# Kernel optimization log

Measured on AMD Instinct MI355X. Metric: run time of the kernel, lower is better.

Reference implementation:

```python
import jax, jax.numpy as jnp
import numpy as np

N = 100_000      # nodes
E = 1_600_000    # edges (avg degree 16)
DN = 64          # node feature dim
DE = 64          # edge feature dim


def _w(k, shape):
    fan_in = shape[0]
    return jax.random.normal(k, shape, dtype=jnp.float32) / np.sqrt(fan_in)


def setup_inputs() -> dict:
    key = jax.random.key(0)
    ks = jax.random.split(key, 12)
    x = jax.random.normal(ks[0], (N, DN), dtype=jnp.float32)
    e = jax.random.normal(ks[1], (E, DE), dtype=jnp.float32)
    senders = jax.random.randint(ks[2], (E,), 0, N)
    receivers = jax.random.randint(ks[3], (E,), 0, N)
    return {
        "x": x, "e": e, "senders": senders, "receivers": receivers,
        "We1": _w(ks[4], (DE + 2 * DN, DE)), "be1": jnp.zeros((DE,), jnp.float32),
        "We2": _w(ks[5], (DE, DE)),          "be2": jnp.zeros((DE,), jnp.float32),
        "We3": _w(ks[6], (DE, DE)),          "be3": jnp.zeros((DE,), jnp.float32),
        "Wn1": _w(ks[7], (DN + DE, DN)),     "bn1": jnp.zeros((DN,), jnp.float32),
        "Wn2": _w(ks[8], (DN, DN)),          "bn2": jnp.zeros((DN,), jnp.float32),
        "Wn3": _w(ks[9], (DN, DN)),          "bn3": jnp.zeros((DN,), jnp.float32),
    }


def reference(x, e, senders, receivers,
              We1, be1, We2, be2, We3, be3,
              Wn1, bn1, Wn2, bn2, Wn3, bn3):
    # --- EdgeBlock: concat(edge, sender, receiver) -> MLP ---
    h = jnp.concatenate([e, x[senders], x[receivers]], axis=-1)  # [E, DE+2*DN]
    h = jax.nn.relu(h @ We1 + be1)
    h = jax.nn.relu(h @ We2 + be2)
    e_new = h @ We3 + be3                                        # [E, DE]
    # --- NodeBlock: sum-aggregate receiving edges, concat(node, agg) -> MLP ---
    agg = jax.ops.segment_sum(e_new, receivers, num_segments=N)  # [N, DE]
    g = jnp.concatenate([x, agg], axis=-1)                       # [N, DN+DE]
    g = jax.nn.relu(g @ Wn1 + bn1)
    g = jax.nn.relu(g @ Wn2 + bn2)
    x_new = g @ Wn3 + bn3                                        # [N, DN]
    return x_new
```

## Files before the change

### kernel.cpp

```cpp
#include <hip/hip_runtime.h>

#define NN 100000
#define NE 1600000

typedef short v8s __attribute__((ext_vector_type(8)));
typedef float v4f __attribute__((ext_vector_type(4)));
typedef unsigned short v4u16 __attribute__((ext_vector_type(4)));

__device__ __forceinline__ unsigned short f2bf(float f) {
    union { float f; unsigned int u; } v; v.f = f;
    unsigned int r = v.u + 0x7FFFu + ((v.u >> 16) & 1u);
    return (unsigned short)(r >> 16);
}

__device__ __forceinline__ void store_bf4(unsigned short* base, int row, int k, float4 v) {
    v4u16 p;
    p.x = f2bf(v.x); p.y = f2bf(v.y); p.z = f2bf(v.z); p.w = f2bf(v.w);
    *(v4u16*)(base + ((k >> 5) * 2048 + row * 32 + (k & 31))) = p;
}

#define MFMA16(acc, a, b) acc = __builtin_amdgcn_mfma_f32_16x16x32_bf16(a, b, acc, 0, 0, 0)

__global__ __launch_bounds__(256, 2) void edge_kernel(
    const float* __restrict__ x, const float* __restrict__ e,
    const int* __restrict__ snd, const int* __restrict__ rcv,
    const float* __restrict__ We1, const float* __restrict__ be1,
    const float* __restrict__ We2, const float* __restrict__ be2,
    const float* __restrict__ We3, const float* __restrict__ be3,
    float* agg, int numTiles)
{
    extern __shared__ unsigned short smem[];
    unsigned short* WT1 = smem;
    unsigned short* WT2 = WT1 + 12288;
    unsigned short* WT3 = WT2 + 4096;
    unsigned short* A   = WT3 + 4096;

    const int tid = threadIdx.x;

    for (int idx = tid; idx < 192 * 64; idx += 256) {
        int k = idx >> 6, n = idx & 63;
        WT1[(k >> 5) * 2048 + n * 32 + (k & 31)] = f2bf(We1[idx]);
    }
    for (int idx = tid; idx < 64 * 64; idx += 256) {
        int k = idx >> 6, n = idx & 63;
        int off = (k >> 5) * 2048 + n * 32 + (k & 31);
        WT2[off] = f2bf(We2[idx]);
        WT3[off] = f2bf(We3[idx]);
    }

    const int lane = tid & 63;
    const int wv   = tid >> 6;
    const int l15  = lane & 15;
    const int quad = lane >> 4;
    const int astrip = wv * 16;

    float b1v[4], b2v[4], b3v[4];
#pragma unroll
    for (int nt = 0; nt < 4; ++nt) {
        b1v[nt] = be1[nt * 16 + l15];
        b2v[nt] = be2[nt * 16 + l15];
        b3v[nt] = be3[nt * 16 + l15];
    }

    const int arow = (astrip + l15) * 32 + quad * 8;
    const int brow = l15 * 32 + quad * 8;

    __syncthreads();

    for (int tile = blockIdx.x; tile < numTiles; tile += gridDim.x) {
        const int ebase = tile * 64;

#pragma unroll
        for (int t = 0; t < 4; ++t) {
            int idx = tid + t * 256;
            int row = idx >> 4;
            int k0  = (idx & 15) * 4;
            float4 ve = *(const float4*)(e + (size_t)(ebase + row) * 64 + k0);
            store_bf4(A, row, k0, ve);
            int s = snd[ebase + row];
            float4 vs = *(const float4*)(x + (size_t)s * 64 + k0);
            store_bf4(A, row, 64 + k0, vs);
            int r = rcv[ebase + row];
            float4 vr = *(const float4*)(x + (size_t)r * 64 + k0);
            store_bf4(A, row, 128 + k0, vr);
        }
        __syncthreads();

        {
            v4f acc[4];
#pragma unroll
            for (int nt = 0; nt < 4; ++nt) acc[nt] = (v4f){0.f, 0.f, 0.f, 0.f};
#pragma unroll
            for (int kb = 0; kb < 6; ++kb) {
                v8s af = *(const v8s*)(A + kb * 2048 + arow);
#pragma unroll
                for (int nt = 0; nt < 4; ++nt) {
                    v8s bf = *(const v8s*)(WT1 + kb * 2048 + brow + nt * 512);
                    MFMA16(acc[nt], af, bf);
                }
            }
#pragma unroll
            for (int nt = 0; nt < 4; ++nt) {
                int kk = nt * 16 + l15;
#pragma unroll
                for (int r = 0; r < 4; ++r) {
                    int m = astrip + quad * 4 + r;
                    float v = acc[nt][r] + b1v[nt];
                    v = v > 0.f ? v : 0.f;
                    A[(kk >> 5) * 2048 + m * 32 + (kk & 31)] = f2bf(v);
                }
            }
        }

        {
            v4f acc[4];
#pragma unroll
            for (int nt = 0; nt < 4; ++nt) acc[nt] = (v4f){0.f, 0.f, 0.f, 0.f};
#pragma unroll
            for (int kb = 0; kb < 2; ++kb) {
                v8s af = *(const v8s*)(A + kb * 2048 + arow);
#pragma unroll
                for (int nt = 0; nt < 4; ++nt) {
                    v8s bf = *(const v8s*)(WT2 + kb * 2048 + brow + nt * 512);
                    MFMA16(acc[nt], af, bf);
                }
            }
#pragma unroll
            for (int nt = 0; nt < 4; ++nt) {
                int kk = nt * 16 + l15;
#pragma unroll
                for (int r = 0; r < 4; ++r) {
                    int m = astrip + quad * 4 + r;
                    float v = acc[nt][r] + b2v[nt];
                    v = v > 0.f ? v : 0.f;
                    A[(2 + (kk >> 5)) * 2048 + m * 32 + (kk & 31)] = f2bf(v);
                }
            }
        }

        {
            v4f acc[4];
#pragma unroll
            for (int nt = 0; nt < 4; ++nt) acc[nt] = (v4f){0.f, 0.f, 0.f, 0.f};
#pragma unroll
            for (int kb = 0; kb < 2; ++kb) {
                v8s af = *(const v8s*)(A + (2 + kb) * 2048 + arow);
#pragma unroll
                for (int nt = 0; nt < 4; ++nt) {
                    v8s bf = *(const v8s*)(WT3 + kb * 2048 + brow + nt * 512);
                    MFMA16(acc[nt], af, bf);
                }
            }
#pragma unroll
            for (int r = 0; r < 4; ++r) {
                int el = astrip + quad * 4 + r;
                int dst = rcv[ebase + el];
                float* aggrow = agg + (size_t)dst * 64;
#pragma unroll
                for (int nt = 0; nt < 4; ++nt) {
                    unsafeAtomicAdd(aggrow + nt * 16 + l15, acc[nt][r] + b3v[nt]);
                }
            }
        }
        __syncthreads();
    }
}

__global__ __launch_bounds__(256, 2) void node_kernel(
    const float* __restrict__ x,
    const float* __restrict__ Wn1, const float* __restrict__ bn1,
    const float* __restrict__ Wn2, const float* __restrict__ bn2,
    const float* __restrict__ Wn3, const float* __restrict__ bn3,
    float* aggout)
{
    extern __shared__ unsigned short smem[];
    unsigned short* WT1 = smem;
    unsigned short* WT2 = WT1 + 8192;
    unsigned short* WT3 = WT2 + 4096;
    unsigned short* A   = WT3 + 4096;

    const int tid = threadIdx.x;

    for (int idx = tid; idx < 128 * 64; idx += 256) {
        int k = idx >> 6, n = idx & 63;
        WT1[(k >> 5) * 2048 + n * 32 + (k & 31)] = f2bf(Wn1[idx]);
    }
    for (int idx = tid; idx < 64 * 64; idx += 256) {
        int k = idx >> 6, n = idx & 63;
        int off = (k >> 5) * 2048 + n * 32 + (k & 31);
        WT2[off] = f2bf(Wn2[idx]);
        WT3[off] = f2bf(Wn3[idx]);
    }

    const int lane = tid & 63;
    const int wv   = tid >> 6;
    const int l15  = lane & 15;
    const int quad = lane >> 4;
    const int astrip = wv * 16;

    float b1v[4], b2v[4], b3v[4];
#pragma unroll
    for (int nt = 0; nt < 4; ++nt) {
        b1v[nt] = bn1[nt * 16 + l15];
        b2v[nt] = bn2[nt * 16 + l15];
        b3v[nt] = bn3[nt * 16 + l15];
    }

    const int arow = (astrip + l15) * 32 + quad * 8;
    const int brow = l15 * 32 + quad * 8;
    const int nbase = blockIdx.x * 64;

    __syncthreads();

#pragma unroll
    for (int t = 0; t < 4; ++t) {
        int idx = tid + t * 256;
        int row = idx >> 4;
        int k0  = (idx & 15) * 4;
        int node = nbase + row;
        float4 vx = {0.f, 0.f, 0.f, 0.f}, va = {0.f, 0.f, 0.f, 0.f};
        if (node < NN) {
            vx = *(const float4*)(x + (size_t)node * 64 + k0);
            va = *(const float4*)(aggout + (size_t)node * 64 + k0);
        }
        store_bf4(A, row, k0, vx);
        store_bf4(A, row, 64 + k0, va);
    }
    __syncthreads();

    {
        v4f acc[4];
#pragma unroll
        for (int nt = 0; nt < 4; ++nt) acc[nt] = (v4f){0.f, 0.f, 0.f, 0.f};
#pragma unroll
        for (int kb = 0; kb < 4; ++kb) {
            v8s af = *(const v8s*)(A + kb * 2048 + arow);
#pragma unroll
            for (int nt = 0; nt < 4; ++nt) {
                v8s bf = *(const v8s*)(WT1 + kb * 2048 + brow + nt * 512);
                MFMA16(acc[nt], af, bf);
            }
        }
#pragma unroll
        for (int nt = 0; nt < 4; ++nt) {
            int kk = nt * 16 + l15;
#pragma unroll
            for (int r = 0; r < 4; ++r) {
                int m = astrip + quad * 4 + r;
                float v = acc[nt][r] + b1v[nt];
                v = v > 0.f ? v : 0.f;
                A[(kk >> 5) * 2048 + m * 32 + (kk & 31)] = f2bf(v);
            }
        }
    }

    {
        v4f acc[4];
#pragma unroll
        for (int nt = 0; nt < 4; ++nt) acc[nt] = (v4f){0.f, 0.f, 0.f, 0.f};
#pragma unroll
        for (int kb = 0; kb < 2; ++kb) {
            v8s af = *(const v8s*)(A + kb * 2048 + arow);
#pragma unroll
            for (int nt = 0; nt < 4; ++nt) {
                v8s bf = *(const v8s*)(WT2 + kb * 2048 + brow + nt * 512);
                MFMA16(acc[nt], af, bf);
            }
        }
#pragma unroll
        for (int nt = 0; nt < 4; ++nt) {
            int kk = nt * 16 + l15;
#pragma unroll
            for (int r = 0; r < 4; ++r) {
                int m = astrip + quad * 4 + r;
                float v = acc[nt][r] + b2v[nt];
                v = v > 0.f ? v : 0.f;
                A[(2 + (kk >> 5)) * 2048 + m * 32 + (kk & 31)] = f2bf(v);
            }
        }
    }

    {
        v4f acc[4];
#pragma unroll
        for (int nt = 0; nt < 4; ++nt) acc[nt] = (v4f){0.f, 0.f, 0.f, 0.f};
#pragma unroll
        for (int kb = 0; kb < 2; ++kb) {
            v8s af = *(const v8s*)(A + (2 + kb) * 2048 + arow);
#pragma unroll
            for (int nt = 0; nt < 4; ++nt) {
                v8s bf = *(const v8s*)(WT3 + kb * 2048 + brow + nt * 512);
                MFMA16(acc[nt], af, bf);
            }
        }
#pragma unroll
        for (int r = 0; r < 4; ++r) {
            int node = nbase + astrip + quad * 4 + r;
            if (node < NN) {
#pragma unroll
                for (int nt = 0; nt < 4; ++nt) {
                    aggout[(size_t)node * 64 + nt * 16 + l15] = acc[nt][r] + b3v[nt];
                }
            }
        }
    }
}

extern "C" void kernel_launch(void* const* d_in, const int* in_sizes, int n_in,
                              void* d_out, int out_size, void* d_ws, size_t ws_size,
                              hipStream_t stream) {
    const float* x   = (const float*)d_in[0];
    const float* e   = (const float*)d_in[1];
    const int*   snd = (const int*)d_in[2];
    const int*   rcv = (const int*)d_in[3];
    const float* We1 = (const float*)d_in[4];  const float* be1 = (const float*)d_in[5];
    const float* We2 = (const float*)d_in[6];  const float* be2 = (const float*)d_in[7];
    const float* We3 = (const float*)d_in[8];  const float* be3 = (const float*)d_in[9];
    const float* Wn1 = (const float*)d_in[10]; const float* bn1 = (const float*)d_in[11];
    const float* Wn2 = (const float*)d_in[12]; const float* bn2 = (const float*)d_in[13];
    const float* Wn3 = (const float*)d_in[14]; const float* bn3 = (const float*)d_in[15];
    float* out = (float*)d_out;

    hipMemsetAsync(out, 0, (size_t)NN * 64 * sizeof(float), stream);

    edge_kernel<<<512, 256, 65536, stream>>>(x, e, snd, rcv,
                                             We1, be1, We2, be2, We3, be3,
                                             out, NE / 64);

    node_kernel<<<(NN + 63) / 64, 256, 49152, stream>>>(x,
                                                        Wn1, bn1, Wn2, bn2, Wn3, bn3,
                                                        out);
}
```

Measured before the change: 874.6 us.

## Sort edges by receiver, swizzle LDS, keep small weights in registers, persistent node kernel

Adds a counting-sort pass (count, single-block scan, fill) that builds a receiver-sorted permutation. The edge kernel walks edges through this permutation and merges runs of equal receivers before issuing atomics, which cuts atomic traffic. LDS tiles get an XOR swizzle to avoid bank conflicts. The 64x64 layer-2/3 weights move into registers to shrink LDS and raise occupancy to 3 blocks. The node kernel becomes persistent. In exchange, edge feature reads are now gathered through the permutation, and the preprocessing adds extra launches, including a serial single-block scan.

```diff
diff --git a/kernel.cpp b/kernel.cpp
--- a/kernel.cpp
+++ b/kernel.cpp
@@ -13,39 +13,76 @@
     return (unsigned short)(r >> 16);
 }
 
+__device__ __forceinline__ int swz_p(int row, int p) {
+    return (p & 7) | (((((p >> 3) ^ (row >> 1))) & 3) << 3);
+}
+
 __device__ __forceinline__ void store_bf4(unsigned short* base, int row, int k, float4 v) {
     v4u16 p;
     p.x = f2bf(v.x); p.y = f2bf(v.y); p.z = f2bf(v.z); p.w = f2bf(v.w);
-    *(v4u16*)(base + ((k >> 5) * 2048 + row * 32 + (k & 31))) = p;
+    *(v4u16*)(base + ((k >> 5) * 2048 + row * 32 + swz_p(row, k & 31))) = p;
 }
 
 #define MFMA16(acc, a, b) acc = __builtin_amdgcn_mfma_f32_16x16x32_bf16(a, b, acc, 0, 0, 0)
 
-__global__ __launch_bounds__(256, 2) void edge_kernel(
+__global__ void count_kernel(const int* __restrict__ rcv, int* cnt) {
+    int i = blockIdx.x * 256 + threadIdx.x;
+    if (i < NE) atomicAdd(&cnt[rcv[i]], 1);
+}
+
+__global__ void scan_kernel(const int* __restrict__ cnt, int* cur) {
+    __shared__ int wsum[16];
+    __shared__ int carry_s;
+    const int tid = threadIdx.x;
+    const int lane = tid & 63, w = tid >> 6;
+    if (tid == 0) carry_s = 0;
+    __syncthreads();
+    for (int base = 0; base < NN; base += 1024) {
+        int i = base + tid;
+        int v = (i < NN) ? cnt[i] : 0;
+        int s = v;
+#pragma unroll
+        for (int off = 1; off < 64; off <<= 1) {
+            int t = __shfl_up(s, off, 64);
+            if (lane >= off) s += t;
+        }
+        if (lane == 63) wsum[w] = s;
+        __syncthreads();
+        int woff = 0;
+        for (int j = 0; j < w; ++j) woff += wsum[j];
+        int carry = carry_s;
+        __syncthreads();
+        if (i < NN) cur[i] = carry + woff + s - v;
+        if (tid == 1023) carry_s = carry + woff + s;
+        __syncthreads();
+    }
+}
+
+__global__ void fill_kernel(const int* __restrict__ rcv, int* cur, int* perm) {
+    int i = blockIdx.x * 256 + threadIdx.x;
+    if (i < NE) {
+        int p = atomicAdd(&cur[rcv[i]], 1);
+        perm[p] = i;
+    }
+}
+
+__global__ __launch_bounds__(256, 3) void edge_kernel(
     const float* __restrict__ x, const float* __restrict__ e,
     const int* __restrict__ snd, const int* __restrict__ rcv,
     const float* __restrict__ We1, const float* __restrict__ be1,
     const float* __restrict__ We2, const float* __restrict__ be2,
     const float* __restrict__ We3, const float* __restrict__ be3,
-    float* agg, int numTiles)
+    const int* __restrict__ perm, float* agg, int numTiles)
 {
     extern __shared__ unsigned short smem[];
     unsigned short* WT1 = smem;
-    unsigned short* WT2 = WT1 + 12288;
-    unsigned short* WT3 = WT2 + 4096;
-    unsigned short* A   = WT3 + 4096;
+    unsigned short* A   = smem + 12288;
 
     const int tid = threadIdx.x;
 
     for (int idx = tid; idx < 192 * 64; idx += 256) {
         int k = idx >> 6, n = idx & 63;
-        WT1[(k >> 5) * 2048 + n * 32 + (k & 31)] = f2bf(We1[idx]);
-    }
-    for (int idx = tid; idx < 64 * 64; idx += 256) {
-        int k = idx >> 6, n = idx & 63;
-        int off = (k >> 5) * 2048 + n * 32 + (k & 31);
-        WT2[off] = f2bf(We2[idx]);
-        WT3[off] = f2bf(We3[idx]);
+        WT1[(k >> 5) * 2048 + n * 32 + swz_p(n, k & 31)] = f2bf(We1[idx]);
     }
 
     const int lane = tid & 63;
@@ -54,6 +91,23 @@
     const int quad = lane >> 4;
     const int astrip = wv * 16;
 
+    v8s w2f[2][4], w3f[2][4];
+#pragma unroll
+    for (int kb = 0; kb < 2; ++kb)
+#pragma unroll
+        for (int nt = 0; nt < 4; ++nt) {
+            int n = nt * 16 + l15;
+            v8s f2, f3;
+#pragma unroll
+            for (int j = 0; j < 8; ++j) {
+                int k = kb * 32 + quad * 8 + j;
+                f2[j] = (short)f2bf(We2[k * 64 + n]);
+                f3[j] = (short)f2bf(We3[k * 64 + n]);
+            }
+            w2f[kb][nt] = f2;
+            w3f[kb][nt] = f3;
+        }
+
     float b1v[4], b2v[4], b3v[4];
 #pragma unroll
     for (int nt = 0; nt < 4; ++nt) {
@@ -62,8 +116,14 @@
         b3v[nt] = be3[nt * 16 + l15];
     }
 
-    const int arow = (astrip + l15) * 32 + quad * 8;
-    const int brow = l15 * 32 + quad * 8;
+    const int amrow = astrip + l15;
+    const int aoff  = amrow * 32 + (((quad ^ (amrow >> 1)) & 3) << 3);
+    int boff[4];
+#pragma unroll
+    for (int nt = 0; nt < 4; ++nt) {
+        int n = nt * 16 + l15;
+        boff[nt] = n * 32 + (((quad ^ (n >> 1)) & 3) << 3);
+    }
 
     __syncthreads();
 
@@ -75,12 +135,13 @@
             int idx = tid + t * 256;
             int row = idx >> 4;
             int k0  = (idx & 15) * 4;
-            float4 ve = *(const float4*)(e + (size_t)(ebase + row) * 64 + k0);
+            int eid = perm ? perm[ebase + row] : (ebase + row);
+            float4 ve = *(const float4*)(e + (size_t)eid * 64 + k0);
             store_bf4(A, row, k0, ve);
-            int s = snd[ebase + row];
+            int s = snd[eid];
             float4 vs = *(const float4*)(x + (size_t)s * 64 + k0);
             store_bf4(A, row, 64 + k0, vs);
-            int r = rcv[ebase + row];
+            int r = rcv[eid];
             float4 vr = *(const float4*)(x + (size_t)r * 64 + k0);
             store_bf4(A, row, 128 + k0, vr);
         }
@@ -92,10 +153,10 @@
             for (int nt = 0; nt < 4; ++nt) acc[nt] = (v4f){0.f, 0.f, 0.f, 0.f};
 #pragma unroll
             for (int kb = 0; kb < 6; ++kb) {
-                v8s af = *(const v8s*)(A + kb * 2048 + arow);
+                v8s af = *(const v8s*)(A + kb * 2048 + aoff);
 #pragma unroll
                 for (int nt = 0; nt < 4; ++nt) {
-                    v8s bf = *(const v8s*)(WT1 + kb * 2048 + brow + nt * 512);
+                    v8s bf = *(const v8s*)(WT1 + kb * 2048 + boff[nt]);
                     MFMA16(acc[nt], af, bf);
                 }
             }
@@ -107,7 +168,7 @@
                     int m = astrip + quad * 4 + r;
                     float v = acc[nt][r] + b1v[nt];
                     v = v > 0.f ? v : 0.f;
-                    A[(kk >> 5) * 2048 + m * 32 + (kk & 31)] = f2bf(v);
+                    A[(kk >> 5) * 2048 + m * 32 + swz_p(m, kk & 31)] = f2bf(v);
                 }
             }
         }
@@ -118,12 +179,9 @@
             for (int nt = 0; nt < 4; ++nt) acc[nt] = (v4f){0.f, 0.f, 0.f, 0.f};
 #pragma unroll
             for (int kb = 0; kb < 2; ++kb) {
-                v8s af = *(const v8s*)(A + kb * 2048 + arow);
-#pragma unroll
-                for (int nt = 0; nt < 4; ++nt) {
-                    v8s bf = *(const v8s*)(WT2 + kb * 2048 + brow + nt * 512);
-                    MFMA16(acc[nt], af, bf);
-                }
+                v8s af = *(const v8s*)(A + kb * 2048 + aoff);
+#pragma unroll
+                for (int nt = 0; nt < 4; ++nt) MFMA16(acc[nt], af, w2f[kb][nt]);
             }
 #pragma unroll
             for (int nt = 0; nt < 4; ++nt) {
@@ -133,7 +191,7 @@
                     int m = astrip + quad * 4 + r;
                     float v = acc[nt][r] + b2v[nt];
                     v = v > 0.f ? v : 0.f;
-                    A[(2 + (kk >> 5)) * 2048 + m * 32 + (kk & 31)] = f2bf(v);
+                    A[(2 + (kk >> 5)) * 2048 + m * 32 + swz_p(m, kk & 31)] = f2bf(v);
                 }
             }
         }
@@ -144,52 +202,61 @@
             for (int nt = 0; nt < 4; ++nt) acc[nt] = (v4f){0.f, 0.f, 0.f, 0.f};
 #pragma unroll
             for (int kb = 0; kb < 2; ++kb) {
-                v8s af = *(const v8s*)(A + (2 + kb) * 2048 + arow);
-#pragma unroll
-                for (int nt = 0; nt < 4; ++nt) {
-                    v8s bf = *(const v8s*)(WT3 + kb * 2048 + brow + nt * 512);
-                    MFMA16(acc[nt], af, bf);
-                }
-            }
+                v8s af = *(const v8s*)(A + (2 + kb) * 2048 + aoff);
+#pragma unroll
+                for (int nt = 0; nt < 4; ++nt) MFMA16(acc[nt], af, w3f[kb][nt]);
+            }
+            int dsts[4];
 #pragma unroll
             for (int r = 0; r < 4; ++r) {
                 int el = astrip + quad * 4 + r;
-                int dst = rcv[ebase + el];
-                float* aggrow = agg + (size_t)dst * 64;
-#pragma unroll
-                for (int nt = 0; nt < 4; ++nt) {
-                    unsafeAtomicAdd(aggrow + nt * 16 + l15, acc[nt][r] + b3v[nt]);
-                }
-            }
-        }
-        __syncthreads();
-    }
-}
-
-__global__ __launch_bounds__(256, 2) void node_kernel(
+                int eid = perm ? perm[ebase + el] : (ebase + el);
+                dsts[r] = rcv[eid];
+            }
+            float sum[4];
+            int cur = dsts[0];
+#pragma unroll
+            for (int nt = 0; nt < 4; ++nt) sum[nt] = acc[nt][0] + b3v[nt];
+#pragma unroll
+            for (int r = 1; r < 4; ++r) {
+                if (dsts[r] == cur) {
+#pragma unroll
+                    for (int nt = 0; nt < 4; ++nt) sum[nt] += acc[nt][r] + b3v[nt];
+                } else {
+                    float* aggrow = agg + (size_t)cur * 64;
+#pragma unroll
+                    for (int nt = 0; nt < 4; ++nt)
+                        unsafeAtomicAdd(aggrow + nt * 16 + l15, sum[nt]);
+                    cur = dsts[r];
+#pragma unroll
+                    for (int nt = 0; nt < 4; ++nt) sum[nt] = acc[nt][r] + b3v[nt];
+                }
+            }
+            float* aggrow = agg + (size_t)cur * 64;
+#pragma unroll
+            for (int nt = 0; nt < 4; ++nt)
+                unsafeAtomicAdd(aggrow + nt * 16 + l15, sum[nt]);
+        }
+        __syncthreads();
+    }
+}
+
+__global__ __launch_bounds__(256, 3) void node_kernel(
     const float* __restrict__ x,
     const float* __restrict__ Wn1, const float* __restrict__ bn1,
     const float* __restrict__ Wn2, const float* __restrict__ bn2,
     const float* __restrict__ Wn3, const float* __restrict__ bn3,
-    float* aggout)
+    float* aggout, int numTiles)
 {
     extern __shared__ unsigned short smem[];
     unsigned short* WT1 = smem;
-    unsigned short* WT2 = WT1 + 8192;
-    unsigned short* WT3 = WT2 + 4096;
-    unsigned short* A   = WT3 + 4096;
+    unsigned short* A   = smem + 8192;
 
     const int tid = threadIdx.x;
 
     for (int idx = tid; idx < 128 * 64; idx += 256) {
         int k = idx >> 6, n = idx & 63;
-        WT1[(k >> 5) * 2048 + n * 32 + (k & 31)] = f2bf(Wn1[idx]);
-    }
-    for (int idx = tid; idx < 64 * 64; idx += 256) {
-        int k = idx >> 6, n = idx & 63;
-        int off = (k >> 5) * 2048 + n * 32 + (k & 31);
-        WT2[off] = f2bf(Wn2[idx]);
-        WT3[off] = f2bf(Wn3[idx]);
+        WT1[(k >> 5) * 2048 + n * 32 + swz_p(n, k & 31)] = f2bf(Wn1[idx]);
     }
 
     const int lane = tid & 63;
@@ -198,6 +265,23 @@
     const int quad = lane >> 4;
     const int astrip = wv * 16;
 
+    v8s w2f[2][4], w3f[2][4];
+#pragma unroll
+    for (int kb = 0; kb < 2; ++kb)
+#pragma unroll
+        for (int nt = 0; nt < 4; ++nt) {
+            int n = nt * 16 + l15;
+            v8s f2, f3;
+#pragma unroll
+            for (int j = 0; j < 8; ++j) {
+                int k = kb * 32 + quad * 8 + j;
+                f2[j] = (short)f2bf(Wn2[k * 64 + n]);
+                f3[j] = (short)f2bf(Wn3[k * 64 + n]);
+            }
+            w2f[kb][nt] = f2;
+            w3f[kb][nt] = f3;
+        }
+
     float b1v[4], b2v[4], b3v[4];
 #pragma unroll
     for (int nt = 0; nt < 4; ++nt) {
@@ -206,103 +290,106 @@
         b3v[nt] = bn3[nt * 16 + l15];
     }
 
-    const int arow = (astrip + l15) * 32 + quad * 8;
-    const int brow = l15 * 32 + quad * 8;
-    const int nbase = blockIdx.x * 64;
+    const int amrow = astrip + l15;
+    const int aoff  = amrow * 32 + (((quad ^ (amrow >> 1)) & 3) << 3);
+    int boff[4];
+#pragma unroll
+    for (int nt = 0; nt < 4; ++nt) {
+        int n = nt * 16 + l15;
+        boff[nt] = n * 32 + (((quad ^ (n >> 1)) & 3) << 3);
+    }
 
     __syncthreads();
 
-#pragma unroll
-    for (int t = 0; t < 4; ++t) {
-        int idx = tid + t * 256;
-        int row = idx >> 4;
-        int k0  = (idx & 15) * 4;
-        int node = nbase + row;
-        float4 vx = {0.f, 0.f, 0.f, 0.f}, va = {0.f, 0.f, 0.f, 0.f};
-        if (node < NN) {
-            vx = *(const float4*)(x + (size_t)node * 64 + k0);
-            va = *(const float4*)(aggout + (size_t)node * 64 + k0);
-        }
-        store_bf4(A, row, k0, vx);
-        store_bf4(A, row, 64 + k0, va);
-    }
-    __syncthreads();
-
-    {
-        v4f acc[4];
-#pragma unroll
-        for (int nt = 0; nt < 4; ++nt) acc[nt] = (v4f){0.f, 0.f, 0.f, 0.f};
-#pragma unroll
-        for (int kb = 0; kb < 4; ++kb) {
-            v8s af = *(const v8s*)(A + kb * 2048 + arow);
+    for (int tile = blockIdx.x; tile < numTiles; tile += gridDim.x) {
+        const int nbase = tile * 64;
+
+#pragma unroll
+        for (int t = 0; t < 4; ++t) {
+            int idx = tid + t * 256;
+            int row = idx >> 4;
+            int k0  = (idx & 15) * 4;
+            int node = nbase + row;
+            float4 vx = {0.f, 0.f, 0.f, 0.f}, va = {0.f, 0.f, 0.f, 0.f};
+            if (node < NN) {
+                vx = *(const float4*)(x + (size_t)node * 64 + k0);
+                va = *(const float4*)(aggout + (size_t)node * 64 + k0);
+            }
+            store_bf4(A, row, k0, vx);
+            store_bf4(A, row, 64 + k0, va);
+        }
+        __syncthreads();
+
+        {
+            v4f acc[4];
+#pragma unroll
+            for (int nt = 0; nt < 4; ++nt) acc[nt] = (v4f){0.f, 0.f, 0.f, 0.f};
+#pragma unroll
+            for (int kb = 0; kb < 4; ++kb) {
+                v8s af = *(const v8s*)(A + kb * 2048 + aoff);
+#pragma unroll
+                for (int nt = 0; nt < 4; ++nt) {
+                    v8s bf = *(const v8s*)(WT1 + kb * 2048 + boff[nt]);
+                    MFMA16(acc[nt], af, bf);
+                }
+            }
 #pragma unroll
             for (int nt = 0; nt < 4; ++nt) {
-                v8s bf = *(const v8s*)(WT1 + kb * 2048 + brow + nt * 512);
-                MFMA16(acc[nt], af, bf);
-            }
-        }
-#pragma unroll
-        for (int nt = 0; nt < 4; ++nt) {
-            int kk = nt * 16 + l15;
+                int kk = nt * 16 + l15;
+#pragma unroll
+                for (int r = 0; r < 4; ++r) {
+                    int m = astrip + quad * 4 + r;
+                    float v = acc[nt][r] + b1v[nt];
+                    v = v > 0.f ? v : 0.f;
+                    A[(kk >> 5) * 2048 + m * 32 + swz_p(m, kk & 31)] = f2bf(v);
+                }
+            }
+        }
+
+        {
+            v4f acc[4];
+#pragma unroll
+            for (int nt = 0; nt < 4; ++nt) acc[nt] = (v4f){0.f, 0.f, 0.f, 0.f};
+#pragma unroll
+            for (int kb = 0; kb < 2; ++kb) {
+                v8s af = *(const v8s*)(A + kb * 2048 + aoff);
+#pragma unroll
+                for (int nt = 0; nt < 4; ++nt) MFMA16(acc[nt], af, w2f[kb][nt]);
+            }
+#pragma unroll
+            for (int nt = 0; nt < 4; ++nt) {
+                int kk = nt * 16 + l15;
+#pragma unroll
+                for (int r = 0; r < 4; ++r) {
+                    int m = astrip + quad * 4 + r;
+                    float v = acc[nt][r] + b2v[nt];
+                    v = v > 0.f ? v : 0.f;
+                    A[(2 + (kk >> 5)) * 2048 + m * 32 + swz_p(m, kk & 31)] = f2bf(v);
+                }
+            }
+        }
+
+        {
+            v4f acc[4];
+#pragma unroll
+            for (int nt = 0; nt < 4; ++nt) acc[nt] = (v4f){0.f, 0.f, 0.f, 0.f};
+#pragma unroll
+            for (int kb = 0; kb < 2; ++kb) {
+                v8s af = *(const v8s*)(A + (2 + kb) * 2048 + aoff);
+#pragma unroll
+                for (int nt = 0; nt < 4; ++nt) MFMA16(acc[nt], af, w3f[kb][nt]);
+            }
 #pragma unroll
             for (int r = 0; r < 4; ++r) {
-                int m = astrip + quad * 4 + r;
-                float v = acc[nt][r] + b1v[nt];
-                v = v > 0.f ? v : 0.f;
-                A[(kk >> 5) * 2048 + m * 32 + (kk & 31)] = f2bf(v);
-            }
-        }
-    }
-
-    {
-        v4f acc[4];
-#pragma unroll
-        for (int nt = 0; nt < 4; ++nt) acc[nt] = (v4f){0.f, 0.f, 0.f, 0.f};
-#pragma unroll
-        for (int kb = 0; kb < 2; ++kb) {
-            v8s af = *(const v8s*)(A + kb * 2048 + arow);
-#pragma unroll
-            for (int nt = 0; nt < 4; ++nt) {
-                v8s bf = *(const v8s*)(WT2 + kb * 2048 + brow + nt * 512);
-                MFMA16(acc[nt], af, bf);
-            }
-        }
-#pragma unroll
-        for (int nt = 0; nt < 4; ++nt) {
-            int kk = nt * 16 + l15;
-#pragma unroll
-            for (int r = 0; r < 4; ++r) {
-                int m = astrip + quad * 4 + r;
-                float v = acc[nt][r] + b2v[nt];
-                v = v > 0.f ? v : 0.f;
-                A[(2 + (kk >> 5)) * 2048 + m * 32 + (kk & 31)] = f2bf(v);
-            }
-        }
-    }
-
-    {
-        v4f acc[4];
-#pragma unroll
-        for (int nt = 0; nt < 4; ++nt) acc[nt] = (v4f){0.f, 0.f, 0.f, 0.f};
-#pragma unroll
-        for (int kb = 0; kb < 2; ++kb) {
-            v8s af = *(const v8s*)(A + (2 + kb) * 2048 + arow);
-#pragma unroll
-            for (int nt = 0; nt < 4; ++nt) {
-                v8s bf = *(const v8s*)(WT3 + kb * 2048 + brow + nt * 512);
-                MFMA16(acc[nt], af, bf);
-            }
-        }
-#pragma unroll
-        for (int r = 0; r < 4; ++r) {
-            int node = nbase + astrip + quad * 4 + r;
-            if (node < NN) {
-#pragma unroll
-                for (int nt = 0; nt < 4; ++nt) {
-                    aggout[(size_t)node * 64 + nt * 16 + l15] = acc[nt][r] + b3v[nt];
-                }
-            }
-        }
+                int node = nbase + astrip + quad * 4 + r;
+                if (node < NN) {
+#pragma unroll
+                    for (int nt = 0; nt < 4; ++nt)
+                        aggout[(size_t)node * 64 + nt * 16 + l15] = acc[nt][r] + b3v[nt];
+                }
+            }
+        }
+        __syncthreads();
     }
 }
 
@@ -323,11 +410,23 @@
 
     hipMemsetAsync(out, 0, (size_t)NN * 64 * sizeof(float), stream);
 
-    edge_kernel<<<512, 256, 65536, stream>>>(x, e, snd, rcv,
+    const size_t need = (size_t)(2 * NN + NE) * sizeof(int);
+    int* perm = nullptr;
+    if (ws_size >= need) {
+        int* cnt = (int*)d_ws;
+        int* cur = cnt + NN;
+        perm     = cur + NN;
+        hipMemsetAsync(cnt, 0, (size_t)NN * sizeof(int), stream);
+        count_kernel<<<(NE + 255) / 256, 256, 0, stream>>>(rcv, cnt);
+        scan_kernel<<<1, 1024, 0, stream>>>(cnt, cur);
+        fill_kernel<<<(NE + 255) / 256, 256, 0, stream>>>(rcv, cur, perm);
+    }
+
+    edge_kernel<<<768, 256, 49152, stream>>>(x, e, snd, rcv,
                                              We1, be1, We2, be2, We3, be3,
-                                             out, NE / 64);
-
-    node_kernel<<<(NN + 63) / 64, 256, 49152, stream>>>(x,
-                                                        Wn1, bn1, Wn2, bn2, Wn3, bn3,
-                                                        out);
-}
+                                             perm, out, NE / 64);
+
+    node_kernel<<<512, 256, 32768, stream>>>(x,
+                                             Wn1, bn1, Wn2, bn2, Wn3, bn3,
+                                             out, (NN + 63) / 64);
+}
```

Result: slower. 1.237 ms (+41.4%).
